# Performance work log

Hardware: AMD Instinct MI355X
Metric: run time of the kernel (lower is better)

## Reference

```python
import jax, jax.numpy as jnp
import numpy as np

N = 50000      # nodes
E = 1600000    # edges
IN_DIM = 64
H = 8          # num_heads
D = 8          # out_dim per head


def setup_inputs() -> dict:
    key = jax.random.key(0)
    ks = jax.random.split(key, 12)
    scale = 1.0 / np.sqrt(IN_DIM)
    inp = {
        "h": jax.random.normal(ks[0], (N, IN_DIM), jnp.float32),
        "e": jax.random.normal(ks[1], (E, IN_DIM), jnp.float32),
        "Wq": jax.random.normal(ks[2], (IN_DIM, H * D), jnp.float32) * scale,
        "bq": jnp.zeros((H * D,), jnp.float32),
        "Wk": jax.random.normal(ks[3], (IN_DIM, H * D), jnp.float32) * scale,
        "bk": jnp.zeros((H * D,), jnp.float32),
        "Wv": jax.random.normal(ks[4], (IN_DIM, H * D), jnp.float32) * scale,
        "bv": jnp.zeros((H * D,), jnp.float32),
        "We": jax.random.normal(ks[5], (IN_DIM, H * D), jnp.float32) * scale,
        "be": jnp.zeros((H * D,), jnp.float32),
        "src": jax.random.randint(ks[6], (E,), 0, N, jnp.int32),
        "dst": jax.random.randint(ks[7], (E,), 0, N, jnp.int32),
    }
    return inp


def reference(h, e, Wq, bq, Wk, bk, Wv, bv, We, be, src, dst):
    n = h.shape[0]
    # Node projections -> [N, H, D]; edge projection -> [E, H, D]
    Q = (h @ Wq + bq).reshape(n, H, D)
    K = (h @ Wk + bk).reshape(n, H, D)
    V = (h @ Wv + bv).reshape(n, H, D)
    pe = (e @ We + be).reshape(-1, H, D)

    inv_sqrt_d = jnp.float32(1.0 / np.sqrt(D))
    # edge-wise: K[src] * Q[dst] / sqrt(D) * proj_e
    score = K[src] * Q[dst] * inv_sqrt_d * pe          # [E, H, D]
    e_out = score                                       # edge output (pre-exp)
    # clamped exp of per-head sum -> [E, H, 1]
    s = jnp.exp(jnp.clip(jnp.sum(score, axis=-1, keepdims=True), -5.0, 5.0))

    # aggregate to destination nodes (DGL recv side)
    wV = jax.ops.segment_sum(V[src] * s, dst, num_segments=n)   # [N, H, D]
    z = jax.ops.segment_sum(s, dst, num_segments=n)             # [N, H, 1]
    h_out = wV / (z + jnp.float32(1e-6))
    return h_out, e_out
```

## Files before the change

kernel.cpp:

```cpp
#include <hip/hip_runtime.h>


using short8 = __attribute__((ext_vector_type(8))) short;
using f32x16 = __attribute__((ext_vector_type(16))) float;

__device__ __forceinline__ short f2bf(float f) {
    unsigned u = __builtin_bit_cast(unsigned, f);
    u += 0x7FFF + ((u >> 16) & 1);
    return (short)(u >> 16);
}

__global__ __launch_bounds__(256)
void proj_kernel(const float* __restrict__ hsrc,
                 const float* __restrict__ Wq, const float* __restrict__ bq,
                 const float* __restrict__ Wk, const float* __restrict__ bk,
                 const float* __restrict__ Wv, const float* __restrict__ bv,
                 float* __restrict__ Q, float* __restrict__ K, float* __restrict__ V,
                 int n)
{
    const float* W;
    const float* b;
    float* out;
    if (blockIdx.y == 0)      { W = Wq; b = bq; out = Q; }
    else if (blockIdx.y == 1) { W = Wk; b = bk; out = K; }
    else                      { W = Wv; b = bv; out = V; }

    const int t    = threadIdx.x;
    const int lane = t & 63;
    const int w    = t >> 6;

    float wcol[64];
#pragma unroll
    for (int k = 0; k < 64; ++k) wcol[k] = W[k * 64 + lane];
    const float bias = b[lane];

    __shared__ float4 sh[16][16];
    const float4* __restrict__ h4 = (const float4*)hsrc;

    const int ngroups = (n + 15) >> 4;
    for (int g = blockIdx.x; g < ngroups; g += gridDim.x) {
        const int base = g << 4;
        {
            const int rs = t >> 4, c4 = t & 15;
            float4 v = make_float4(0.f, 0.f, 0.f, 0.f);
            if (base + rs < n) v = h4[(size_t)(base + rs) * 16 + c4];
            __syncthreads();
            sh[rs][c4] = v;
            __syncthreads();
        }
        float acc0 = bias, acc1 = bias, acc2 = bias, acc3 = bias;
#pragma unroll
        for (int k4 = 0; k4 < 16; ++k4) {
            const float w0 = wcol[k4 * 4 + 0], w1 = wcol[k4 * 4 + 1];
            const float w2 = wcol[k4 * 4 + 2], w3 = wcol[k4 * 4 + 3];
            const float4 a = sh[w * 4 + 0][k4];
            const float4 bb = sh[w * 4 + 1][k4];
            const float4 c = sh[w * 4 + 2][k4];
            const float4 d = sh[w * 4 + 3][k4];
            acc0 = fmaf(a.w,  w3, fmaf(a.z,  w2, fmaf(a.y,  w1, fmaf(a.x,  w0, acc0))));
            acc1 = fmaf(bb.w, w3, fmaf(bb.z, w2, fmaf(bb.y, w1, fmaf(bb.x, w0, acc1))));
            acc2 = fmaf(c.w,  w3, fmaf(c.z,  w2, fmaf(c.y,  w1, fmaf(c.x,  w0, acc2))));
            acc3 = fmaf(d.w,  w3, fmaf(d.z,  w2, fmaf(d.y,  w1, fmaf(d.x,  w0, acc3))));
        }
        const int n0 = base + w * 4;
        if (n0 + 0 < n) out[(size_t)(n0 + 0) * 64 + lane] = acc0;
        if (n0 + 1 < n) out[(size_t)(n0 + 1) * 64 + lane] = acc1;
        if (n0 + 2 < n) out[(size_t)(n0 + 2) * 64 + lane] = acc2;
        if (n0 + 3 < n) out[(size_t)(n0 + 3) * 64 + lane] = acc3;
    }
}

__global__ __launch_bounds__(256)
void rank_kernel(const int* __restrict__ dst, int* __restrict__ counts,
                 int* __restrict__ rank, int E)
{
    int i = blockIdx.x * 256 + threadIdx.x;
    const int stride = gridDim.x * 256;
    for (; i < E; i += stride) {
        rank[i] = atomicAdd(&counts[dst[i]], 1);
    }
}

__global__ __launch_bounds__(1024)
void scan1_kernel(const int* __restrict__ counts, int* __restrict__ offsets,
                  int* __restrict__ bsum, int n)
{
    const int t = threadIdx.x;
    const int lane = t & 63;
    const int w = t >> 6;
    __shared__ int wsum[16];
    const int i = blockIdx.x * 1024 + t;
    const int v = (i < n) ? counts[i] : 0;
    int x = v;
#pragma unroll
    for (int d = 1; d < 64; d <<= 1) {
        int y = __shfl_up(x, d);
        if (lane >= d) x += y;
    }
    if (lane == 63) wsum[w] = x;
    __syncthreads();
    if (w == 0 && lane < 16) {
        int s = wsum[lane];
#pragma unroll
        for (int d = 1; d < 16; d <<= 1) {
            int y = __shfl_up(s, d);
            if (lane >= d) s += y;
        }
        wsum[lane] = s;
    }
    __syncthreads();
    const int excl = ((w == 0) ? 0 : wsum[w - 1]) + (x - v);
    if (i < n) offsets[i] = excl;
    if (t == 1023) bsum[blockIdx.x] = excl + v;
}

__global__ __launch_bounds__(64)
void scan2_kernel(int* __restrict__ bsum, int nb)
{
    const int lane = threadIdx.x;
    const int v = (lane < nb) ? bsum[lane] : 0;
    int x = v;
#pragma unroll
    for (int d = 1; d < 64; d <<= 1) {
        int y = __shfl_up(x, d);
        if (lane >= d) x += y;
    }
    if (lane < nb) bsum[lane] = x - v;
}

__global__ __launch_bounds__(1024)
void scan3_kernel(int* __restrict__ offsets, const int* __restrict__ bsum,
                  int n, int E)
{
    const int i = blockIdx.x * 1024 + threadIdx.x;
    if (i < n) offsets[i] += bsum[blockIdx.x];
    if (blockIdx.x == 0 && threadIdx.x == 0) offsets[n] = E;
}

__global__ __launch_bounds__(256)
void edge_kernel(const float* __restrict__ e,
                 const float* __restrict__ We, const float* __restrict__ be,
                 const int* __restrict__ src, const int* __restrict__ dst,
                 const float* __restrict__ Q, const float* __restrict__ K,
                 float* __restrict__ e_out,
                 float* __restrict__ s_sorted, int* __restrict__ src_sorted,
                 const int* __restrict__ rank, const int* __restrict__ offs,
                 int E)
{
    __shared__ float4 tile4[4][32 * 8];
    const int t    = threadIdx.x;
    const int lane = t & 63;
    const int wu   = __builtin_amdgcn_readfirstlane(t >> 6);
    const int lid  = lane & 31;
    const int hi   = lane >> 5;
    float4* const myT4 = tile4[wu];
    const float inv = 0.35355339059327373f;

    short8 Afr[2][4];
#pragma unroll
    for (int jh = 0; jh < 2; ++jh)
#pragma unroll
        for (int ks = 0; ks < 4; ++ks)
#pragma unroll
            for (int g = 0; g < 2; ++g)
#pragma unroll
                for (int i = 0; i < 4; ++i)
                    Afr[jh][ks][4 * g + i] =
                        f2bf(We[(16 * ks + 8 * g + 4 * hi + i) * 64 + 32 * jh + lid]);

    const int ntiles = (E + 63) >> 6;
    for (int tb = blockIdx.x * 4 + wu; tb < ntiles; tb += gridDim.x * 4) {
        const int base = tb << 6;

#pragma unroll
        for (int eh = 0; eh < 2; ++eh) {
            const int erow_i = base + eh * 32 + lid;
            const int erc = erow_i < E ? erow_i : (E - 1);
            const int se = src[erc];
            const int de = dst[erc];
            const int rk = offs[de] + rank[erc];

            const float* er = e + (size_t)erc * 64 + 4 * hi;
            short8 Bfr[4];
#pragma unroll
            for (int ks = 0; ks < 4; ++ks) {
                const float4 p0 = *(const float4*)(er + 16 * ks);
                const float4 p1 = *(const float4*)(er + 16 * ks + 8);
                Bfr[ks][0] = f2bf(p0.x); Bfr[ks][1] = f2bf(p0.y);
                Bfr[ks][2] = f2bf(p0.z); Bfr[ks][3] = f2bf(p0.w);
                Bfr[ks][4] = f2bf(p1.x); Bfr[ks][5] = f2bf(p1.y);
                Bfr[ks][6] = f2bf(p1.z); Bfr[ks][7] = f2bf(p1.w);
            }

            float gate[8];
#pragma unroll
            for (int jh = 0; jh < 2; ++jh) {
                f32x16 D = {};
#pragma unroll
                for (int ks = 0; ks < 4; ++ks)
                    D = __builtin_amdgcn_mfma_f32_32x32x16_bf16(
                            Afr[jh][ks], Bfr[ks], D, 0, 0, 0);

                asm volatile("s_waitcnt lgkmcnt(0)" ::: "memory");

                const float* kb = K + (size_t)se * 64 + 32 * jh + 4 * hi;
                const float* qb = Q + (size_t)de * 64 + 32 * jh + 4 * hi;
#pragma unroll
                for (int hd = 0; hd < 4; ++hd) {
                    const float4 kv  = *(const float4*)(kb + 8 * hd);
                    const float4 qv  = *(const float4*)(qb + 8 * hd);
                    const float4 bev = *(const float4*)(be + 32 * jh + 8 * hd + 4 * hi);
                    const float s0 = kv.x * qv.x * inv * (D[4 * hd + 0] + bev.x);
                    const float s1 = kv.y * qv.y * inv * (D[4 * hd + 1] + bev.y);
                    const float s2 = kv.z * qv.z * inv * (D[4 * hd + 2] + bev.z);
                    const float s3 = kv.w * qv.w * inv * (D[4 * hd + 3] + bev.w);
                    const int c4 = (2 * hd + hi) ^ (lid & 7);
                    myT4[lid * 8 + c4] = make_float4(s0, s1, s2, s3);
                    float p = (s0 + s1) + (s2 + s3);
                    const float full = p + __shfl_xor(p, 32);
                    gate[jh * 4 + hd] = expf(fminf(fmaxf(full, -5.f), 5.f));
                }

                const int r8 = lane >> 3, m = lane & 7;
#pragma unroll
                for (int it = 0; it < 4; ++it) {
                    const int row = it * 8 + r8;
                    const int edge2 = base + eh * 32 + row;
                    const float4 v = myT4[row * 8 + (m ^ (row & 7))];
                    if (edge2 < E)
                        *((float4*)e_out + (size_t)edge2 * 16 + jh * 8 + m) = v;
                }
            }

            if (erow_i < E) {
                const float4 g = (hi == 0)
                    ? make_float4(gate[0], gate[1], gate[2], gate[3])
                    : make_float4(gate[4], gate[5], gate[6], gate[7]);
                *(float4*)(s_sorted + (size_t)rk * 8 + hi * 4) = g;
                if (hi == 0) src_sorted[rk] = se;
            }
        }
    }
}

__global__ __launch_bounds__(256)
void aggregate_kernel(const int* __restrict__ offsets,
                      const int* __restrict__ src_sorted,
                      const float* __restrict__ s_sorted,
                      const float* __restrict__ V,
                      float* __restrict__ hout, int n)
{
    const int w = (blockIdx.x * 256 + threadIdx.x) >> 6;
    const int lane = threadIdx.x & 63;
    if (w >= n) return;
    const int o0 = offsets[w], o1 = offsets[w + 1];
    const int head = lane >> 3;
    float acc = 0.f, zacc = 0.f;
    int j = o0;
    for (; j + 4 <= o1; j += 4) {
        const int sv0 = src_sorted[j + 0];
        const int sv1 = src_sorted[j + 1];
        const int sv2 = src_sorted[j + 2];
        const int sv3 = src_sorted[j + 3];
        const float s0 = s_sorted[(size_t)(j + 0) * 8 + head];
        const float s1 = s_sorted[(size_t)(j + 1) * 8 + head];
        const float s2 = s_sorted[(size_t)(j + 2) * 8 + head];
        const float s3 = s_sorted[(size_t)(j + 3) * 8 + head];
        const float v0 = V[(size_t)sv0 * 64 + lane];
        const float v1 = V[(size_t)sv1 * 64 + lane];
        const float v2 = V[(size_t)sv2 * 64 + lane];
        const float v3 = V[(size_t)sv3 * 64 + lane];
        acc = fmaf(v0, s0, acc);
        acc = fmaf(v1, s1, acc);
        acc = fmaf(v2, s2, acc);
        acc = fmaf(v3, s3, acc);
        zacc += (s0 + s1) + (s2 + s3);
    }
    for (; j < o1; ++j) {
        const int sv = src_sorted[j];
        const float s = s_sorted[(size_t)j * 8 + head];
        acc = fmaf(V[(size_t)sv * 64 + lane], s, acc);
        zacc += s;
    }
    hout[(size_t)w * 64 + lane] = acc / (zacc + 1e-6f);
}

extern "C" void kernel_launch(void* const* d_in, const int* in_sizes, int n_in,
                              void* d_out, int out_size, void* d_ws, size_t ws_size,
                              hipStream_t stream)
{
    const float* h  = (const float*)d_in[0];
    const float* e  = (const float*)d_in[1];
    const float* Wq = (const float*)d_in[2];
    const float* bq = (const float*)d_in[3];
    const float* Wk = (const float*)d_in[4];
    const float* bk = (const float*)d_in[5];
    const float* Wv = (const float*)d_in[6];
    const float* bv = (const float*)d_in[7];
    const float* We = (const float*)d_in[8];
    const float* be = (const float*)d_in[9];
    const int* src  = (const int*)d_in[10];
    const int* dst  = (const int*)d_in[11];

    const int N = in_sizes[0] / 64;
    const int E = in_sizes[1] / 64;

    float* hout  = (float*)d_out;
    float* e_out = (float*)d_out + (size_t)N * 64;

    char* ws = (char*)d_ws;
    float* Q = (float*)ws;                 ws += (size_t)N * 64 * sizeof(float);
    float* K = (float*)ws;                 ws += (size_t)N * 64 * sizeof(float);
    float* V = (float*)ws;                 ws += (size_t)N * 64 * sizeof(float);
    float* s_sorted = (float*)ws;          ws += (size_t)E * 8 * sizeof(float);
    int* src_sorted = (int*)ws;            ws += (size_t)E * sizeof(int);
    int* rank = (int*)ws;                  ws += (size_t)E * sizeof(int);
    int* counts  = (int*)ws;               ws += (size_t)N * sizeof(int);
    int* offsets = (int*)ws;               ws += (size_t)(N + 1) * sizeof(int);
    int* bsum    = (int*)ws;               ws += 64 * sizeof(int);

    hipMemsetAsync(counts, 0, (size_t)N * sizeof(int), stream);

    proj_kernel<<<dim3(512, 3), dim3(256), 0, stream>>>(
        h, Wq, bq, Wk, bk, Wv, bv, Q, K, V, N);

    rank_kernel<<<dim3(2048), dim3(256), 0, stream>>>(dst, counts, rank, E);

    const int nb = (N + 1023) / 1024;
    scan1_kernel<<<dim3(nb), dim3(1024), 0, stream>>>(counts, offsets, bsum, N);
    scan2_kernel<<<dim3(1), dim3(64), 0, stream>>>(bsum, nb);
    scan3_kernel<<<dim3(nb), dim3(1024), 0, stream>>>(offsets, bsum, N, E);

    const int ntiles = (E + 63) >> 6;
    const int eblocks = (ntiles + 3) / 4;
    edge_kernel<<<dim3(eblocks), dim3(256), 0, stream>>>(
        e, We, be, src, dst, Q, K, e_out, s_sorted, src_sorted, rank, offsets, E);

    const int ablocks = (N * 64 + 255) / 256;
    aggregate_kernel<<<dim3(ablocks), dim3(256), 0, stream>>>(
        offsets, src_sorted, s_sorted, V, hout, N);
}
```

Measured before the change: 569.9 us.

## Software-pipeline edge kernel with prefetch of next 32-edge unit and persistent grid

Rewrites the edge kernel loop to process 32-edge units with register double-buffering: the next unit's src/dst/rank and edge feature rows are loaded before computing the current unit, with a sched_barrier to keep loads issued early. The grid is changed from one block per 4 tiles to a fixed 2048 persistent blocks striding over units. This aims to hide global load latency of the streaming edge features behind MFMA and gather work, at the cost of more live registers (16 extra float4) which may reduce occupancy.

Result: slower. 616.0 us (+8.1%).

```diff
diff --git a/kernel.cpp b/kernel.cpp
--- a/kernel.cpp
+++ b/kernel.cpp
@@ -137,6 +137,17 @@
     if (blockIdx.x == 0 && threadIdx.x == 0) offsets[n] = E;
 }
 
+#define LOAD_UNIT(U, SE, DE, RK, P0,P1,P2,P3,P4,P5,P6,P7) do {            \
+    const int _erow = (U) * 32 + lid;                                      \
+    const int _erc  = _erow < E ? _erow : (E - 1);                         \
+    SE = src[_erc]; DE = dst[_erc]; RK = rank[_erc];                       \
+    const float* _er = e + (size_t)_erc * 64 + 4 * hi;                     \
+    P0 = *(const float4*)(_er + 0);  P1 = *(const float4*)(_er + 8);       \
+    P2 = *(const float4*)(_er + 16); P3 = *(const float4*)(_er + 24);      \
+    P4 = *(const float4*)(_er + 32); P5 = *(const float4*)(_er + 40);      \
+    P6 = *(const float4*)(_er + 48); P7 = *(const float4*)(_er + 56);      \
+} while (0)
+
 __global__ __launch_bounds__(256)
 void edge_kernel(const float* __restrict__ e,
                  const float* __restrict__ We, const float* __restrict__ be,
@@ -168,78 +179,91 @@
                     Afr[jh][ks][4 * g + i] =
                         f2bf(We[(16 * ks + 8 * g + 4 * hi + i) * 64 + 32 * jh + lid]);
 
-    const int ntiles = (E + 63) >> 6;
-    for (int tb = blockIdx.x * 4 + wu; tb < ntiles; tb += gridDim.x * 4) {
-        const int base = tb << 6;
-
-#pragma unroll
-        for (int eh = 0; eh < 2; ++eh) {
-            const int erow_i = base + eh * 32 + lid;
-            const int erc = erow_i < E ? erow_i : (E - 1);
-            const int se = src[erc];
-            const int de = dst[erc];
-            const int rk = offs[de] + rank[erc];
-
-            const float* er = e + (size_t)erc * 64 + 4 * hi;
-            short8 Bfr[4];
-#pragma unroll
-            for (int ks = 0; ks < 4; ++ks) {
-                const float4 p0 = *(const float4*)(er + 16 * ks);
-                const float4 p1 = *(const float4*)(er + 16 * ks + 8);
-                Bfr[ks][0] = f2bf(p0.x); Bfr[ks][1] = f2bf(p0.y);
-                Bfr[ks][2] = f2bf(p0.z); Bfr[ks][3] = f2bf(p0.w);
-                Bfr[ks][4] = f2bf(p1.x); Bfr[ks][5] = f2bf(p1.y);
-                Bfr[ks][6] = f2bf(p1.z); Bfr[ks][7] = f2bf(p1.w);
+    const int nunits  = (E + 31) >> 5;
+    const int wstride = gridDim.x * 4;
+    int u = blockIdx.x * 4 + wu;
+    if (u >= nunits) return;
+
+    int se, de, rkr;
+    float4 p0, p1, p2, p3, p4, p5, p6, p7;
+    LOAD_UNIT(u, se, de, rkr, p0, p1, p2, p3, p4, p5, p6, p7);
+
+    for (;;) {
+        const int un = u + wstride;
+        const int uc = un < nunits ? un : u;
+        int se_n, de_n, rk_n;
+        float4 n0, n1, n2, n3, n4, n5, n6, n7;
+        LOAD_UNIT(uc, se_n, de_n, rk_n, n0, n1, n2, n3, n4, n5, n6, n7);
+        __builtin_amdgcn_sched_barrier(0);
+
+        const int base32 = u * 32;
+        const int erow   = base32 + lid;
+        const bool valid = erow < E;
+        const int rk = offs[de] + rkr;
+
+        short8 Bfr[4];
+#pragma unroll
+        for (int ks = 0; ks < 4; ++ks) {
+            const float4 pa = (ks == 0) ? p0 : (ks == 1) ? p2 : (ks == 2) ? p4 : p6;
+            const float4 pb = (ks == 0) ? p1 : (ks == 1) ? p3 : (ks == 2) ? p5 : p7;
+            Bfr[ks][0] = f2bf(pa.x); Bfr[ks][1] = f2bf(pa.y);
+            Bfr[ks][2] = f2bf(pa.z); Bfr[ks][3] = f2bf(pa.w);
+            Bfr[ks][4] = f2bf(pb.x); Bfr[ks][5] = f2bf(pb.y);
+            Bfr[ks][6] = f2bf(pb.z); Bfr[ks][7] = f2bf(pb.w);
+        }
+
+        float gate[8];
+#pragma unroll
+        for (int jh = 0; jh < 2; ++jh) {
+            f32x16 D = {};
+#pragma unroll
+            for (int ks = 0; ks < 4; ++ks)
+                D = __builtin_amdgcn_mfma_f32_32x32x16_bf16(
+                        Afr[jh][ks], Bfr[ks], D, 0, 0, 0);
+
+            asm volatile("s_waitcnt lgkmcnt(0)" ::: "memory");
+
+            const float* kb = K + (size_t)se * 64 + 32 * jh + 4 * hi;
+            const float* qb = Q + (size_t)de * 64 + 32 * jh + 4 * hi;
+#pragma unroll
+            for (int hd = 0; hd < 4; ++hd) {
+                const float4 kv  = *(const float4*)(kb + 8 * hd);
+                const float4 qv  = *(const float4*)(qb + 8 * hd);
+                const float4 bev = *(const float4*)(be + 32 * jh + 8 * hd + 4 * hi);
+                const float s0 = kv.x * qv.x * inv * (D[4 * hd + 0] + bev.x);
+                const float s1 = kv.y * qv.y * inv * (D[4 * hd + 1] + bev.y);
+                const float s2 = kv.z * qv.z * inv * (D[4 * hd + 2] + bev.z);
+                const float s3 = kv.w * qv.w * inv * (D[4 * hd + 3] + bev.w);
+                const int c4 = (2 * hd + hi) ^ (lid & 7);
+                myT4[lid * 8 + c4] = make_float4(s0, s1, s2, s3);
+                float pp = (s0 + s1) + (s2 + s3);
+                const float full = pp + __shfl_xor(pp, 32);
+                gate[jh * 4 + hd] = expf(fminf(fmaxf(full, -5.f), 5.f));
             }
 
-            float gate[8];
-#pragma unroll
-            for (int jh = 0; jh < 2; ++jh) {
-                f32x16 D = {};
-#pragma unroll
-                for (int ks = 0; ks < 4; ++ks)
-                    D = __builtin_amdgcn_mfma_f32_32x32x16_bf16(
-                            Afr[jh][ks], Bfr[ks], D, 0, 0, 0);
-
-                asm volatile("s_waitcnt lgkmcnt(0)" ::: "memory");
-
-                const float* kb = K + (size_t)se * 64 + 32 * jh + 4 * hi;
-                const float* qb = Q + (size_t)de * 64 + 32 * jh + 4 * hi;
-#pragma unroll
-                for (int hd = 0; hd < 4; ++hd) {
-                    const float4 kv  = *(const float4*)(kb + 8 * hd);
-                    const float4 qv  = *(const float4*)(qb + 8 * hd);
-                    const float4 bev = *(const float4*)(be + 32 * jh + 8 * hd + 4 * hi);
-                    const float s0 = kv.x * qv.x * inv * (D[4 * hd + 0] + bev.x);
-                    const float s1 = kv.y * qv.y * inv * (D[4 * hd + 1] + bev.y);
-                    const float s2 = kv.z * qv.z * inv * (D[4 * hd + 2] + bev.z);
-                    const float s3 = kv.w * qv.w * inv * (D[4 * hd + 3] + bev.w);
-                    const int c4 = (2 * hd + hi) ^ (lid & 7);
-                    myT4[lid * 8 + c4] = make_float4(s0, s1, s2, s3);
-                    float p = (s0 + s1) + (s2 + s3);
-                    const float full = p + __shfl_xor(p, 32);
-                    gate[jh * 4 + hd] = expf(fminf(fmaxf(full, -5.f), 5.f));
-                }
-
-                const int r8 = lane >> 3, m = lane & 7;
-#pragma unroll
-                for (int it = 0; it < 4; ++it) {
-                    const int row = it * 8 + r8;
-                    const int edge2 = base + eh * 32 + row;
-                    const float4 v = myT4[row * 8 + (m ^ (row & 7))];
-                    if (edge2 < E)
-                        *((float4*)e_out + (size_t)edge2 * 16 + jh * 8 + m) = v;
-                }
+            const int r8 = lane >> 3, m = lane & 7;
+#pragma unroll
+            for (int it = 0; it < 4; ++it) {
+                const int row = it * 8 + r8;
+                const int edge2 = base32 + row;
+                const float4 v = myT4[row * 8 + (m ^ (row & 7))];
+                if (edge2 < E)
+                    *((float4*)e_out + (size_t)edge2 * 16 + jh * 8 + m) = v;
             }
-
-            if (erow_i < E) {
-                const float4 g = (hi == 0)
-                    ? make_float4(gate[0], gate[1], gate[2], gate[3])
-                    : make_float4(gate[4], gate[5], gate[6], gate[7]);
-                *(float4*)(s_sorted + (size_t)rk * 8 + hi * 4) = g;
-                if (hi == 0) src_sorted[rk] = se;
-            }
-        }
+        }
+
+        if (valid) {
+            const float4 g = (hi == 0)
+                ? make_float4(gate[0], gate[1], gate[2], gate[3])
+                : make_float4(gate[4], gate[5], gate[6], gate[7]);
+            *(float4*)(s_sorted + (size_t)rk * 8 + hi * 4) = g;
+            if (hi == 0) src_sorted[rk] = se;
+        }
+
+        if (un >= nunits) break;
+        u = un; se = se_n; de = de_n; rkr = rk_n;
+        p0 = n0; p1 = n1; p2 = n2; p3 = n3;
+        p4 = n4; p5 = n5; p6 = n6; p7 = n7;
     }
 }
 
@@ -331,9 +355,7 @@
     scan2_kernel<<<dim3(1), dim3(64), 0, stream>>>(bsum, nb);
     scan3_kernel<<<dim3(nb), dim3(1024), 0, stream>>>(offsets, bsum, N, E);
 
-    const int ntiles = (E + 63) >> 6;
-    const int eblocks = (ntiles + 3) / 4;
-    edge_kernel<<<dim3(eblocks), dim3(256), 0, stream>>>(
+    edge_kernel<<<dim3(2048), dim3(256), 0, stream>>>(
         e, We, be, src, dst, Q, K, e_out, s_sorted, src_sorted, rank, offsets, E);
 
     const int ablocks = (N * 64 + 255) / 256;
```
